# Optimization experiments

Hardware: AMD Instinct MI355X
Metric: run time of the kernel (lower is better)

## Reference

```python
import jax, jax.numpy as jnp
import numpy as np

N, T, D, H = 32, 2048, 512, 512

def setup_inputs() -> dict:
    key = jax.random.key(0)
    k1, k2, k3, k4 = jax.random.split(key, 4)
    x = jax.random.normal(k1, (N, T, D), dtype=jnp.float32)
    h0 = jax.random.normal(k2, (N, H), dtype=jnp.float32)
    Wx = jax.random.normal(k3, (D, 4 * H), dtype=jnp.float32) / np.sqrt(D)
    Wh = jax.random.normal(k4, (H, 4 * H), dtype=jnp.float32) / np.sqrt(H)
    b = jnp.zeros((4 * H,), dtype=jnp.float32)
    return {"x": x, "h0": h0, "Wx": Wx, "Wh": Wh, "b": b}

def reference(x, h0, Wx, Wh, b):
    # Precompute input contributions for all timesteps: (N, T, 4H)
    xWx = jnp.einsum('ntd,dk->ntk', x, Wx) + b
    c0 = jnp.zeros_like(h0)
    Hd = h0.shape[-1]

    def step(carry, a_x):
        prev_h, prev_c = carry
        a = a_x + prev_h @ Wh  # (N, 4H)
        i = jax.nn.sigmoid(a[:, 0 * Hd:1 * Hd])
        f = jax.nn.sigmoid(a[:, 1 * Hd:2 * Hd])
        o = jax.nn.sigmoid(a[:, 2 * Hd:3 * Hd])
        g = jnp.tanh(a[:, 3 * Hd:4 * Hd])
        next_c = f * prev_c + i * g
        next_h = o * jnp.tanh(next_c)
        return (next_h, next_c), next_h

    # scan over time: move T to leading axis
    _, hs = jax.lax.scan(step, (h0, c0), jnp.swapaxes(xWx, 0, 1))
    return jnp.swapaxes(hs, 0, 1)  # (N, T, H)
```

## Files before the change

### kernel.cpp

```cpp
#include <hip/hip_runtime.h>

typedef __attribute__((ext_vector_type(8))) __bf16 bf16x8;
typedef __attribute__((ext_vector_type(4))) float f32x4;
typedef __attribute__((ext_vector_type(2))) float f32x2;
typedef __attribute__((ext_vector_type(4))) unsigned int u32x4;
typedef unsigned int u32;
typedef unsigned long long u64;

#define NSEQ 32
#define TTOT 2048
#define DIM  512
#define HID  512
#define G4   2048

__device__ __forceinline__ float sigmoidf_(float x) {
    return 1.0f / (1.0f + __expf(-x));
}
__device__ __forceinline__ float tanhf_(float x) {
    return 2.0f / (1.0f + __expf(-2.0f * x)) - 1.0f;
}


__global__ void lstm_init(const float* __restrict__ Wx, const float* __restrict__ Wh,
                          const float* __restrict__ h0,
                          __bf16* __restrict__ WxbT, __bf16* __restrict__ WhbT,
                          __bf16* __restrict__ hcomm, u32* __restrict__ sent,
                          float* __restrict__ cstate)
{
    int idx = blockIdx.x * 256 + threadIdx.x;
    int c = idx & (G4 - 1);
    int k = idx >> 11;
    WxbT[(size_t)c * DIM + k] = (__bf16)Wx[idx];
    WhbT[(size_t)c * HID + k] = (__bf16)Wh[idx];
    if (idx < NSEQ * HID) {
        int seq = idx >> 9, cc = idx & 511;
        int i = seq >> 4, s = seq & 15;
        hcomm[(size_t)i * 8192 + (cc >> 5) * 512 + s * 32 + (cc & 31)] = (__bf16)h0[idx];
        cstate[idx] = 0.0f;
    }
    if (idx < 32) sent[idx] = 0;
}

__global__ __launch_bounds__(256) void gemm_xwx(
    const float* __restrict__ x, const __bf16* __restrict__ WxbT,
    const float* __restrict__ b, float* __restrict__ Axw, int t0, int ltc)
{
    const int Tc   = 1 << ltc;
    const int cb   = blockIdx.x * 128;
    const int m0   = blockIdx.y * 128;
    const int tid  = threadIdx.x;
    const int w    = tid >> 6;
    const int lane = tid & 63;
    const int l15  = lane & 15;
    const int lq   = lane >> 4;
    const int wm   = w >> 1, wn = w & 1;

    f32x4 acc[4][4] = {};

    const float* xrow[4];
#pragma unroll
    for (int mi = 0; mi < 4; ++mi) {
        int r  = m0 + wm * 64 + mi * 16 + l15;
        int n  = r >> ltc;
        int tl = r & (Tc - 1);
        xrow[mi] = x + ((size_t)n * TTOT + (t0 + tl)) * DIM;
    }
    const __bf16* bcol[4];
#pragma unroll
    for (int ni = 0; ni < 4; ++ni)
        bcol[ni] = WxbT + (size_t)(cb + wn * 64 + ni * 16 + l15) * DIM;

    for (int k0 = 0; k0 < DIM; k0 += 32) {
        bf16x8 af[4], bfr[4];
#pragma unroll
        for (int mi = 0; mi < 4; ++mi) {
            const float* p = xrow[mi] + k0 + lq * 8;
            f32x4 f0 = *(const f32x4*)p;
            f32x4 f1 = *(const f32x4*)(p + 4);
            bf16x8 a;
            a[0] = (__bf16)f0[0]; a[1] = (__bf16)f0[1]; a[2] = (__bf16)f0[2]; a[3] = (__bf16)f0[3];
            a[4] = (__bf16)f1[0]; a[5] = (__bf16)f1[1]; a[6] = (__bf16)f1[2]; a[7] = (__bf16)f1[3];
            af[mi] = a;
        }
#pragma unroll
        for (int ni = 0; ni < 4; ++ni)
            bfr[ni] = *(const bf16x8*)(bcol[ni] + k0 + lq * 8);
#pragma unroll
        for (int mi = 0; mi < 4; ++mi)
#pragma unroll
            for (int ni = 0; ni < 4; ++ni)
                acc[mi][ni] = __builtin_amdgcn_mfma_f32_16x16x32_bf16(af[mi], bfr[ni], acc[mi][ni], 0, 0, 0);
    }

#pragma unroll
    for (int ni = 0; ni < 4; ++ni) {
        int col = cb + wn * 64 + ni * 16 + l15;
        float bias = b[col];
#pragma unroll
        for (int mi = 0; mi < 4; ++mi) {
#pragma unroll
            for (int j = 0; j < 4; ++j) {
                int r  = m0 + wm * 64 + mi * 16 + lq * 4 + j;
                int n  = r >> ltc;
                int tl = r & (Tc - 1);
                Axw[((size_t)n * Tc + tl) * G4 + col] = acc[mi][ni][j] + bias;
            }
        }
    }
}

__global__ __launch_bounds__(256, 1) void lstm_rec(
    const float* __restrict__ Axw,
    const __bf16* __restrict__ WhbT,
    __bf16* __restrict__ hcomm,
    u32* __restrict__ sent,
    float* __restrict__ cstate,
    float* __restrict__ out,
    int t0, int Tc)
{
    const int g    = blockIdx.x;
    const int i    = g >> 4;
    const int j    = g & 15;
    const int tid  = threadIdx.x;
    const int w    = tid >> 6;
    const int lane = tid & 63;
    const int l15  = lane & 15;
    const int lq   = lane >> 4;

    bf16x8 bfrag[8][4];
#pragma unroll
    for (int n = 0; n < 8; ++n) {
        const __bf16* base = WhbT
            + (size_t)((n >> 1) * 512 + j * 32 + (n & 1) * 16 + l15) * HID
            + (4 * w) * 32 + lq * 8;
#pragma unroll
        for (int kk = 0; kk < 4; ++kk)
            bfrag[n][kk] = *(const bf16x8*)(base + kk * 32);
    }
#pragma unroll
    for (int n = 0; n < 8; ++n)
#pragma unroll
        for (int kk = 0; kk < 4; ++kk)
            asm volatile("" : "+v"(bfrag[n][kk]));

    const int s   = tid >> 4;
    const int cp  = tid & 15;
    const int seq = i * 16 + s;
    const int hc0 = j * 32 + 2 * cp;
    float c0 = cstate[seq * HID + hc0];
    float c1 = cstate[seq * HID + hc0 + 1];

    const u32* sent_row = sent + i * 16;

    __shared__ float P[4][16][132];

    for (int t = t0; t < t0 + Tc; ++t) {
        const float* Ap = Axw + ((size_t)seq * Tc + (t - t0)) * G4 + hc0;
        f32x2 ax0 = *(const f32x2*)(Ap);
        f32x2 ax1 = *(const f32x2*)(Ap + 512);
        f32x2 ax2 = *(const f32x2*)(Ap + 1024);
        f32x2 ax3 = *(const f32x2*)(Ap + 1536);

        {
            int sv;
            do {
                sv = (int)__hip_atomic_load(&sent_row[lane & 15], __ATOMIC_RELAXED,
                                            __HIP_MEMORY_SCOPE_AGENT);
            } while (!__all(sv >= t));
        }
        __builtin_amdgcn_sched_barrier(0);

        const u64* slotr = (const u64*)hcomm + (size_t)(t & 7) * 4096 + (size_t)i * 2048;
        u64 d[4][2];
#pragma unroll
        for (int kk = 0; kk < 4; ++kk) {
            const u64* p = slotr + (size_t)(4 * w + kk) * 128 + l15 * 8 + lq * 2;
            d[kk][0] = __hip_atomic_load(p,     __ATOMIC_RELAXED, __HIP_MEMORY_SCOPE_AGENT);
            d[kk][1] = __hip_atomic_load(p + 1, __ATOMIC_RELAXED, __HIP_MEMORY_SCOPE_AGENT);
        }

        f32x4 acc[8] = {};
#pragma unroll
        for (int kk = 0; kk < 4; ++kk) {
            u32x4 q = { (u32)d[kk][0], (u32)(d[kk][0] >> 32),
                        (u32)d[kk][1], (u32)(d[kk][1] >> 32) };
            bf16x8 a = __builtin_bit_cast(bf16x8, q);
#pragma unroll
            for (int n = 0; n < 8; ++n)
                acc[n] = __builtin_amdgcn_mfma_f32_16x16x32_bf16(a, bfrag[n][kk], acc[n], 0, 0, 0);
        }

#pragma unroll
        for (int n = 0; n < 8; ++n)
#pragma unroll
            for (int jj = 0; jj < 4; ++jj)
                P[w][lq * 4 + jj][n * 16 + l15] = acc[n][jj];
        __syncthreads();

        f32x2 sq[4];
#pragma unroll
        for (int q = 0; q < 4; ++q) {
            f32x2 v0 = *(const f32x2*)&P[0][s][q * 32 + 2 * cp];
            f32x2 v1 = *(const f32x2*)&P[1][s][q * 32 + 2 * cp];
            f32x2 v2 = *(const f32x2*)&P[2][s][q * 32 + 2 * cp];
            f32x2 v3 = *(const f32x2*)&P[3][s][q * 32 + 2 * cp];
            sq[q].x = (v0.x + v1.x) + (v2.x + v3.x);
            sq[q].y = (v0.y + v1.y) + (v2.y + v3.y);
        }

        float i0 = sigmoidf_(sq[0].x + ax0.x), f0 = sigmoidf_(sq[1].x + ax1.x);
        float o0 = sigmoidf_(sq[2].x + ax2.x), g0 = tanhf_(sq[3].x + ax3.x);
        c0 = f0 * c0 + i0 * g0;
        float h0v = o0 * tanhf_(c0);
        float i1 = sigmoidf_(sq[0].y + ax0.y), f1 = sigmoidf_(sq[1].y + ax1.y);
        float o1 = sigmoidf_(sq[2].y + ax2.y), g1 = tanhf_(sq[3].y + ax3.y);
        c1 = f1 * c1 + i1 * g1;
        float h1v = o1 * tanhf_(c1);

        *(f32x2*)(out + ((size_t)seq * TTOT + t) * HID + hc0) = (f32x2){h0v, h1v};

        {
            u32 v01 = (u32)__builtin_bit_cast(unsigned short, (__bf16)h0v)
                    | ((u32)__builtin_bit_cast(unsigned short, (__bf16)h1v) << 16);
            u32 partner = (u32)__shfl_xor((int)v01, 1);
            if (!(cp & 1)) {
                u64 pk = (u64)v01 | ((u64)partner << 32);
                u64* dst = (u64*)hcomm + (size_t)((t + 1) & 7) * 4096
                         + (size_t)i * 2048 + (size_t)j * 128 + s * 8 + (cp >> 1);
                __hip_atomic_exchange(dst, pk, __ATOMIC_RELAXED, __HIP_MEMORY_SCOPE_AGENT);
            }
        }
        __syncthreads();
        if (tid == 0)
            __hip_atomic_exchange((u32*)&sent_row[j], (u32)(t + 1),
                                  __ATOMIC_RELAXED, __HIP_MEMORY_SCOPE_AGENT);
    }

    cstate[seq * HID + hc0]     = c0;
    cstate[seq * HID + hc0 + 1] = c1;
}

extern "C" void kernel_launch(void* const* d_in, const int* in_sizes, int n_in,
                              void* d_out, int out_size, void* d_ws, size_t ws_size,
                              hipStream_t stream)
{
    const float* x  = (const float*)d_in[0];
    const float* h0 = (const float*)d_in[1];
    const float* Wx = (const float*)d_in[2];
    const float* Wh = (const float*)d_in[3];
    const float* b  = (const float*)d_in[4];
    float* out = (float*)d_out;

    char* ws = (char*)d_ws;
    __bf16* WxbT   = (__bf16*)(ws);
    __bf16* WhbT   = (__bf16*)(ws + (2u << 20));
    __bf16* hcomm  = (__bf16*)(ws + (4u << 20));
    u32*    sent   = (u32*)(ws + (4u << 20) + (256u << 10));
    float*  cstate = (float*)(ws + (4u << 20) + (320u << 10));
    float*  Axw    = (float*)(ws + (4u << 20) + (384u << 10));
    const size_t base = (4u << 20) + (384u << 10);

    int ltc = 11;
    while (ltc > 4 && base + (((size_t)NSEQ << ltc) * G4 * sizeof(float)) > ws_size) --ltc;
    const int Tc = 1 << ltc;

    lstm_init<<<dim3((G4 * DIM) / 256), dim3(256), 0, stream>>>(
        Wx, Wh, h0, WxbT, WhbT, hcomm, sent, cstate);

    for (int t0 = 0; t0 < TTOT; t0 += Tc) {
        gemm_xwx<<<dim3(G4 / 128, (NSEQ << ltc) / 128), dim3(256), 0, stream>>>(
            x, WxbT, b, Axw, t0, ltc);
        lstm_rec<<<dim3(32), dim3(256), 0, stream>>>(
            Axw, WhbT, hcomm, sent, cstate, out, t0, Tc);
    }
}
```

Before: 6.517 ms.

## Fuse input GEMM and recurrence into one persistent kernel with per-timestep flags

Replaces the separate input-projection GEMM and recurrent kernels with a single launch. 32 blocks run the recurrence while 224 blocks compute x·Wx tiles in time order and signal completion through per-timestep counters, so the projection overlaps the serial scan. The projected activations are stored as bf16, which halves their traffic but costs precision. Per-wave sent flags replace the block-wide barrier, and the shared buffer is double-buffered to remove the second __syncthreads. The design relies on all 256 blocks being co-resident, and it adds polling on the done counters.

```diff
diff --git a/kernel.cpp b/kernel.cpp
--- a/kernel.cpp
+++ b/kernel.cpp
@@ -12,6 +12,11 @@
 #define DIM  512
 #define HID  512
 #define G4   2048
+#define NGEMM 224
+#define NTILE 8192
+
+#define AL(p)     __hip_atomic_load((p), __ATOMIC_RELAXED, __HIP_MEMORY_SCOPE_AGENT)
+#define AX(p, v)  __hip_atomic_exchange((p), (v), __ATOMIC_RELAXED, __HIP_MEMORY_SCOPE_AGENT)
 
 __device__ __forceinline__ float sigmoidf_(float x) {
     return 1.0f / (1.0f + __expf(-x));
@@ -19,13 +24,15 @@
 __device__ __forceinline__ float tanhf_(float x) {
     return 2.0f / (1.0f + __expf(-2.0f * x)) - 1.0f;
 }
+__device__ __forceinline__ float bflo(u32 v) { return __builtin_bit_cast(float, v << 16); }
+__device__ __forceinline__ float bfhi(u32 v) { return __builtin_bit_cast(float, v & 0xffff0000u); }
 
 
 __global__ void lstm_init(const float* __restrict__ Wx, const float* __restrict__ Wh,
                           const float* __restrict__ h0,
                           __bf16* __restrict__ WxbT, __bf16* __restrict__ WhbT,
                           __bf16* __restrict__ hcomm, u32* __restrict__ sent,
-                          float* __restrict__ cstate)
+                          u32* __restrict__ doneT, float* __restrict__ cstate)
 {
     int idx = blockIdx.x * 256 + threadIdx.x;
     int c = idx & (G4 - 1);
@@ -38,94 +45,103 @@
         hcomm[(size_t)i * 8192 + (cc >> 5) * 512 + s * 32 + (cc & 31)] = (__bf16)h0[idx];
         cstate[idx] = 0.0f;
     }
-    if (idx < 32) sent[idx] = 0;
-}
-
-__global__ __launch_bounds__(256) void gemm_xwx(
-    const float* __restrict__ x, const __bf16* __restrict__ WxbT,
-    const float* __restrict__ b, float* __restrict__ Axw, int t0, int ltc)
+    if (idx < 128) sent[idx] = 0;
+    if (idx < 512) doneT[idx] = 0;
+}
+
+__global__ __launch_bounds__(256, 1) void lstm_mono(
+    const float* __restrict__ x,
+    const __bf16* __restrict__ WxbT,
+    const float* __restrict__ bvec,
+    const __bf16* __restrict__ WhbT,
+    __bf16* __restrict__ hcomm,
+    u32* __restrict__ sent,
+    u32* __restrict__ doneT,
+    __bf16* __restrict__ AxwB,
+    float* __restrict__ cstate,
+    float* __restrict__ out)
 {
-    const int Tc   = 1 << ltc;
-    const int cb   = blockIdx.x * 128;
-    const int m0   = blockIdx.y * 128;
+    const int bid  = blockIdx.x;
     const int tid  = threadIdx.x;
     const int w    = tid >> 6;
     const int lane = tid & 63;
     const int l15  = lane & 15;
     const int lq   = lane >> 4;
-    const int wm   = w >> 1, wn = w & 1;
-
-    f32x4 acc[4][4] = {};
-
-    const float* xrow[4];
-#pragma unroll
-    for (int mi = 0; mi < 4; ++mi) {
-        int r  = m0 + wm * 64 + mi * 16 + l15;
-        int n  = r >> ltc;
-        int tl = r & (Tc - 1);
-        xrow[mi] = x + ((size_t)n * TTOT + (t0 + tl)) * DIM;
+
+    __shared__ float P[2][4][16][132];
+
+    if (bid >= 32) {
+        const int wm = w >> 1, wn = w & 1;
+        for (int tile = bid - 32; tile < NTILE; tile += NGEMM) {
+            const int ts = tile >> 4;
+            const int cb = (tile & 15) * 128;
+            const int m0 = ts * 128;
+
+            f32x4 acc[4][4] = {};
+            const float* xrow[4];
+#pragma unroll
+            for (int mi = 0; mi < 4; ++mi) {
+                int r = m0 + wm * 64 + mi * 16 + l15;
+                int t = r >> 5, n = r & 31;
+                xrow[mi] = x + ((size_t)n * TTOT + t) * DIM;
+            }
+            const __bf16* bcol[4];
+#pragma unroll
+            for (int ni = 0; ni < 4; ++ni)
+                bcol[ni] = WxbT + (size_t)(cb + wn * 64 + ni * 16 + l15) * DIM;
+
+            for (int k0 = 0; k0 < DIM; k0 += 32) {
+                bf16x8 af[4], bfr[4];
+#pragma unroll
+                for (int mi = 0; mi < 4; ++mi) {
+                    const float* p = xrow[mi] + k0 + lq * 8;
+                    f32x4 f0 = *(const f32x4*)p;
+                    f32x4 f1 = *(const f32x4*)(p + 4);
+                    bf16x8 a;
+                    a[0] = (__bf16)f0[0]; a[1] = (__bf16)f0[1]; a[2] = (__bf16)f0[2]; a[3] = (__bf16)f0[3];
+                    a[4] = (__bf16)f1[0]; a[5] = (__bf16)f1[1]; a[6] = (__bf16)f1[2]; a[7] = (__bf16)f1[3];
+                    af[mi] = a;
+                }
+#pragma unroll
+                for (int ni = 0; ni < 4; ++ni)
+                    bfr[ni] = *(const bf16x8*)(bcol[ni] + k0 + lq * 8);
+#pragma unroll
+                for (int mi = 0; mi < 4; ++mi)
+#pragma unroll
+                    for (int ni = 0; ni < 4; ++ni)
+                        acc[mi][ni] = __builtin_amdgcn_mfma_f32_16x16x32_bf16(af[mi], bfr[ni], acc[mi][ni], 0, 0, 0);
+            }
+
+#pragma unroll
+            for (int ni = 0; ni < 4; ++ni) {
+                int col = cb + wn * 64 + ni * 16 + l15;
+                float bias = bvec[col];
+#pragma unroll
+                for (int mi = 0; mi < 4; ++mi) {
+#pragma unroll
+                    for (int jj = 0; jj < 4; ++jj) {
+                        int r = m0 + wm * 64 + mi * 16 + lq * 4 + jj;
+                        float f = acc[mi][ni][jj] + bias;
+                        u32 hb  = (u32)__builtin_bit_cast(unsigned short, (__bf16)f);
+                        u32 p01 = hb | ((u32)__shfl_xor((int)hb, 1) << 16);
+                        u32 p23 = (u32)__shfl_xor((int)p01, 2);
+                        if ((l15 & 3) == 0) {
+                            u64 pk = (u64)p01 | ((u64)p23 << 32);
+                            u64* dst = (u64*)AxwB + (((size_t)r * G4 + col) >> 2);
+                            AX(dst, pk);
+                        }
+                    }
+                }
+            }
+            __syncthreads();
+            if (tid == 0)
+                __hip_atomic_fetch_add(&doneT[ts], 1u, __ATOMIC_RELAXED, __HIP_MEMORY_SCOPE_AGENT);
+        }
+        return;
     }
-    const __bf16* bcol[4];
-#pragma unroll
-    for (int ni = 0; ni < 4; ++ni)
-        bcol[ni] = WxbT + (size_t)(cb + wn * 64 + ni * 16 + l15) * DIM;
-
-    for (int k0 = 0; k0 < DIM; k0 += 32) {
-        bf16x8 af[4], bfr[4];
-#pragma unroll
-        for (int mi = 0; mi < 4; ++mi) {
-            const float* p = xrow[mi] + k0 + lq * 8;
-            f32x4 f0 = *(const f32x4*)p;
-            f32x4 f1 = *(const f32x4*)(p + 4);
-            bf16x8 a;
-            a[0] = (__bf16)f0[0]; a[1] = (__bf16)f0[1]; a[2] = (__bf16)f0[2]; a[3] = (__bf16)f0[3];
-            a[4] = (__bf16)f1[0]; a[5] = (__bf16)f1[1]; a[6] = (__bf16)f1[2]; a[7] = (__bf16)f1[3];
-            af[mi] = a;
-        }
-#pragma unroll
-        for (int ni = 0; ni < 4; ++ni)
-            bfr[ni] = *(const bf16x8*)(bcol[ni] + k0 + lq * 8);
-#pragma unroll
-        for (int mi = 0; mi < 4; ++mi)
-#pragma unroll
-            for (int ni = 0; ni < 4; ++ni)
-                acc[mi][ni] = __builtin_amdgcn_mfma_f32_16x16x32_bf16(af[mi], bfr[ni], acc[mi][ni], 0, 0, 0);
-    }
-
-#pragma unroll
-    for (int ni = 0; ni < 4; ++ni) {
-        int col = cb + wn * 64 + ni * 16 + l15;
-        float bias = b[col];
-#pragma unroll
-        for (int mi = 0; mi < 4; ++mi) {
-#pragma unroll
-            for (int j = 0; j < 4; ++j) {
-                int r  = m0 + wm * 64 + mi * 16 + lq * 4 + j;
-                int n  = r >> ltc;
-                int tl = r & (Tc - 1);
-                Axw[((size_t)n * Tc + tl) * G4 + col] = acc[mi][ni][j] + bias;
-            }
-        }
-    }
-}
-
-__global__ __launch_bounds__(256, 1) void lstm_rec(
-    const float* __restrict__ Axw,
-    const __bf16* __restrict__ WhbT,
-    __bf16* __restrict__ hcomm,
-    u32* __restrict__ sent,
-    float* __restrict__ cstate,
-    float* __restrict__ out,
-    int t0, int Tc)
-{
-    const int g    = blockIdx.x;
-    const int i    = g >> 4;
-    const int j    = g & 15;
-    const int tid  = threadIdx.x;
-    const int w    = tid >> 6;
-    const int lane = tid & 63;
-    const int l15  = lane & 15;
-    const int lq   = lane >> 4;
+
+    const int i = bid >> 4;
+    const int j = bid & 15;
 
     bf16x8 bfrag[8][4];
 #pragma unroll
@@ -150,24 +166,36 @@
     float c0 = cstate[seq * HID + hc0];
     float c1 = cstate[seq * HID + hc0 + 1];
 
-    const u32* sent_row = sent + i * 16;
-
-    __shared__ float P[4][16][132];
-
-    for (int t = t0; t < t0 + Tc; ++t) {
-        const float* Ap = Axw + ((size_t)seq * Tc + (t - t0)) * G4 + hc0;
-        f32x2 ax0 = *(const f32x2*)(Ap);
-        f32x2 ax1 = *(const f32x2*)(Ap + 512);
-        f32x2 ax2 = *(const f32x2*)(Ap + 1024);
-        f32x2 ax3 = *(const f32x2*)(Ap + 1536);
+    const u32* sw = sent + i * 64 + 16 * w;
+    int ok_t = -1;
+    u32 pv = 0; int pv_ok = 0;
+
+    for (int t = 0; t < TTOT; ++t) {
+        if (t > ok_t) {
+            u32 dv;
+            do { dv = AL(&doneT[t >> 2]); } while (dv < 16u);
+            ok_t = t | 3;
+            pv_ok = 0;
+            asm volatile("" ::: "memory");
+        }
+
+        const size_t arow = (size_t)(t * 32 + seq) * G4 + hc0;
+        u32 a0 = AL((const u32*)(AxwB + arow));
+        u32 a1 = AL((const u32*)(AxwB + arow + 512));
+        u32 a2 = AL((const u32*)(AxwB + arow + 1024));
+        u32 a3 = AL((const u32*)(AxwB + arow + 1536));
 
         {
-            int sv;
-            do {
-                sv = (int)__hip_atomic_load(&sent_row[lane & 15], __ATOMIC_RELAXED,
-                                            __HIP_MEMORY_SCOPE_AGENT);
-            } while (!__all(sv >= t));
-        }
+            int v0 = (int)AL(&sw[l15]);
+            int v1 = (int)AL(&sw[l15]);
+            int v2 = (int)AL(&sw[l15]);
+            int v3 = (int)AL(&sw[l15]);
+            while (!__all(v0 >= t)) {
+                v0 = v1; v1 = v2; v2 = v3;
+                v3 = (int)AL(&sw[l15]);
+            }
+        }
+        asm volatile("" ::: "memory");
         __builtin_amdgcn_sched_barrier(0);
 
         const u64* slotr = (const u64*)hcomm + (size_t)(t & 7) * 4096 + (size_t)i * 2048;
@@ -175,8 +203,8 @@
 #pragma unroll
         for (int kk = 0; kk < 4; ++kk) {
             const u64* p = slotr + (size_t)(4 * w + kk) * 128 + l15 * 8 + lq * 2;
-            d[kk][0] = __hip_atomic_load(p,     __ATOMIC_RELAXED, __HIP_MEMORY_SCOPE_AGENT);
-            d[kk][1] = __hip_atomic_load(p + 1, __ATOMIC_RELAXED, __HIP_MEMORY_SCOPE_AGENT);
+            d[kk][0] = AL(p);
+            d[kk][1] = AL(p + 1);
         }
 
         f32x4 acc[8] = {};
@@ -190,50 +218,57 @@
                 acc[n] = __builtin_amdgcn_mfma_f32_16x16x32_bf16(a, bfrag[n][kk], acc[n], 0, 0, 0);
         }
 
+        const int par = t & 1;
 #pragma unroll
         for (int n = 0; n < 8; ++n)
 #pragma unroll
             for (int jj = 0; jj < 4; ++jj)
-                P[w][lq * 4 + jj][n * 16 + l15] = acc[n][jj];
+                P[par][w][lq * 4 + jj][n * 16 + l15] = acc[n][jj];
         __syncthreads();
 
         f32x2 sq[4];
 #pragma unroll
         for (int q = 0; q < 4; ++q) {
-            f32x2 v0 = *(const f32x2*)&P[0][s][q * 32 + 2 * cp];
-            f32x2 v1 = *(const f32x2*)&P[1][s][q * 32 + 2 * cp];
-            f32x2 v2 = *(const f32x2*)&P[2][s][q * 32 + 2 * cp];
-            f32x2 v3 = *(const f32x2*)&P[3][s][q * 32 + 2 * cp];
+            f32x2 v0 = *(const f32x2*)&P[par][0][s][q * 32 + 2 * cp];
+            f32x2 v1 = *(const f32x2*)&P[par][1][s][q * 32 + 2 * cp];
+            f32x2 v2 = *(const f32x2*)&P[par][2][s][q * 32 + 2 * cp];
+            f32x2 v3 = *(const f32x2*)&P[par][3][s][q * 32 + 2 * cp];
             sq[q].x = (v0.x + v1.x) + (v2.x + v3.x);
             sq[q].y = (v0.y + v1.y) + (v2.y + v3.y);
         }
 
-        float i0 = sigmoidf_(sq[0].x + ax0.x), f0 = sigmoidf_(sq[1].x + ax1.x);
-        float o0 = sigmoidf_(sq[2].x + ax2.x), g0 = tanhf_(sq[3].x + ax3.x);
+        float i0 = sigmoidf_(sq[0].x + bflo(a0)), f0 = sigmoidf_(sq[1].x + bflo(a1));
+        float o0 = sigmoidf_(sq[2].x + bflo(a2)), g0 = tanhf_(sq[3].x + bflo(a3));
         c0 = f0 * c0 + i0 * g0;
         float h0v = o0 * tanhf_(c0);
-        float i1 = sigmoidf_(sq[0].y + ax0.y), f1 = sigmoidf_(sq[1].y + ax1.y);
-        float o1 = sigmoidf_(sq[2].y + ax2.y), g1 = tanhf_(sq[3].y + ax3.y);
+        float i1 = sigmoidf_(sq[0].y + bfhi(a0)), f1 = sigmoidf_(sq[1].y + bfhi(a1));
+        float o1 = sigmoidf_(sq[2].y + bfhi(a2)), g1 = tanhf_(sq[3].y + bfhi(a3));
         c1 = f1 * c1 + i1 * g1;
         float h1v = o1 * tanhf_(c1);
-
-        *(f32x2*)(out + ((size_t)seq * TTOT + t) * HID + hc0) = (f32x2){h0v, h1v};
 
         {
             u32 v01 = (u32)__builtin_bit_cast(unsigned short, (__bf16)h0v)
                     | ((u32)__builtin_bit_cast(unsigned short, (__bf16)h1v) << 16);
-            u32 partner = (u32)__shfl_xor((int)v01, 1);
+            u32 prt = (u32)__shfl_xor((int)v01, 1);
             if (!(cp & 1)) {
-                u64 pk = (u64)v01 | ((u64)partner << 32);
+                u64 pk = (u64)v01 | ((u64)prt << 32);
                 u64* dst = (u64*)hcomm + (size_t)((t + 1) & 7) * 4096
                          + (size_t)i * 2048 + (size_t)j * 128 + s * 8 + (cp >> 1);
-                __hip_atomic_exchange(dst, pk, __ATOMIC_RELAXED, __HIP_MEMORY_SCOPE_AGENT);
-            }
-        }
-        __syncthreads();
-        if (tid == 0)
-            __hip_atomic_exchange((u32*)&sent_row[j], (u32)(t + 1),
-                                  __ATOMIC_RELAXED, __HIP_MEMORY_SCOPE_AGENT);
+                AX(dst, pk);
+            }
+        }
+        asm volatile("s_waitcnt vmcnt(0)" ::: "memory");
+        if (lane == 0)
+            AX(&sent[i * 64 + j * 4 + w], (u32)(t + 1));
+
+        *(f32x2*)(out + ((size_t)seq * TTOT + t) * HID + hc0) = (f32x2){h0v, h1v};
+
+        if (pv_ok && pv >= 16u) ok_t += 4;
+        {
+            int ns = (ok_t + 1) >> 2;
+            if (ns < 512) { pv = AL(&doneT[ns]); pv_ok = 1; }
+            else pv_ok = 0;
+        }
     }
 
     cstate[seq * HID + hc0]     = c0;
@@ -256,21 +291,13 @@
     __bf16* WhbT   = (__bf16*)(ws + (2u << 20));
     __bf16* hcomm  = (__bf16*)(ws + (4u << 20));
     u32*    sent   = (u32*)(ws + (4u << 20) + (256u << 10));
-    float*  cstate = (float*)(ws + (4u << 20) + (320u << 10));
-    float*  Axw    = (float*)(ws + (4u << 20) + (384u << 10));
-    const size_t base = (4u << 20) + (384u << 10);
-
-    int ltc = 11;
-    while (ltc > 4 && base + (((size_t)NSEQ << ltc) * G4 * sizeof(float)) > ws_size) --ltc;
-    const int Tc = 1 << ltc;
+    u32*    doneT  = (u32*)(ws + (4u << 20) + (257u << 10));
+    float*  cstate = (float*)(ws + (4u << 20) + (260u << 10));
+    __bf16* AxwB   = (__bf16*)(ws + (4u << 20) + (512u << 10));
 
     lstm_init<<<dim3((G4 * DIM) / 256), dim3(256), 0, stream>>>(
-        Wx, Wh, h0, WxbT, WhbT, hcomm, sent, cstate);
-
-    for (int t0 = 0; t0 < TTOT; t0 += Tc) {
-        gemm_xwx<<<dim3(G4 / 128, (NSEQ << ltc) / 128), dim3(256), 0, stream>>>(
-            x, WxbT, b, Axw, t0, ltc);
-        lstm_rec<<<dim3(32), dim3(256), 0, stream>>>(
-            Axw, WhbT, hcomm, sent, cstate, out, t0, Tc);
-    }
-}
+        Wx, Wh, h0, WxbT, WhbT, hcomm, sent, doneT, cstate);
+
+    lstm_mono<<<dim3(32 + NGEMM), dim3(256), 0, stream>>>(
+        x, WxbT, b, WhbT, hcomm, sent, doneT, AxwB, cstate, out);
+}
```

After: 7.525 ms. +15.5%, slower.
